# Optimization experiments

Measured on AMD Instinct MI355X. Metric: run time of the kernel, lower is better.

## Reference

```python
import jax, jax.numpy as jnp
import numpy as np


def setup_inputs() -> dict:
    key = jax.random.key(0)
    ks = jax.random.split(key, 6)
    B, S, D = 2048, 50, 128
    H, L = 8, 128
    return {
        "x": jax.random.normal(ks[0], (B, S, D), dtype=jnp.float32),
        "Wq": jax.random.normal(ks[1], (H, D, L), dtype=jnp.float32),
        "Wk": jax.random.normal(ks[2], (H, D, L), dtype=jnp.float32),
        "Wv": jax.random.normal(ks[3], (H, D, L), dtype=jnp.float32),
        "Ws": jax.random.normal(ks[4], (H, L), dtype=jnp.float32),
        "O": jax.random.normal(ks[5], (H * L, D), dtype=jnp.float32),
    }


def reference(x, Wq, Wk, Wv, Ws, O):
    # x: [B, S, D]; origin is the first node of each walk.
    B, S, D = x.shape
    H, _, L = Wq.shape
    origin = x[:, 0, :]  # [B, D]
    # key projection of origin is constant over the sequence -> compute once.
    k = jax.nn.sigmoid(jnp.einsum("bd,hdl->bhl", origin, Wk))  # [B, H, L]
    q = jax.nn.sigmoid(jnp.einsum("bsd,hdl->bshl", x, Wq))      # [B, S, H, L]
    v = jax.nn.sigmoid(jnp.einsum("bsd,hdl->bshl", x, Wv))      # [B, S, H, L]
    edge = k[:, None, :, :] * q                                  # [B, S, H, L]
    score = jnp.einsum("bshl,hl->bsh", edge, Ws)                 # [B, S, H]
    attn = jax.nn.softmax(score, axis=1)                         # softmax over walk positions
    res = jnp.einsum("bsh,bshl->bhl", attn, v)                   # [B, H, L]
    res = res.reshape(B, H * L)                                  # head-major concat (matches tf.concat)
    out = jax.nn.sigmoid(res @ O) + origin                       # [B, D]
    return out
```

## Files before the change

kernel.cpp:

```cpp
#include <hip/hip_runtime.h>
#include <hip/hip_bf16.h>


typedef _Float16 f16x8 __attribute__((ext_vector_type(8)));
typedef float f32x4 __attribute__((ext_vector_type(4)));

#define LOG2E 1.44269504088896340736f

__device__ __forceinline__ unsigned short f2h(float f) {
  _Float16 h = (_Float16)f;
  return __builtin_bit_cast(unsigned short, h);
}
__device__ __forceinline__ float h2f(unsigned short s) {
  return (float)__builtin_bit_cast(_Float16, s);
}
__device__ __forceinline__ float fexp2(float x) {
#if __has_builtin(__builtin_amdgcn_exp2f)
  return __builtin_amdgcn_exp2f(x);
#else
  return exp2f(x);
#endif
}
__device__ __forceinline__ float frcp(float x) {
#if __has_builtin(__builtin_amdgcn_rcpf)
  return __builtin_amdgcn_rcpf(x);
#else
  return 1.0f / x;
#endif
}
__device__ __forceinline__ float sig_scaled(float a) {
  return frcp(1.0f + fexp2(a));
}

__device__ __forceinline__ void dma16(const void* g, void* l) {
  __builtin_amdgcn_global_load_lds(
      (const __attribute__((address_space(1))) unsigned int*)g,
      (__attribute__((address_space(3))) unsigned int*)(unsigned int)(unsigned long long)l,
      16, 0, 0);
}

__global__ void prep_kernel(const float* __restrict__ Wq, const float* __restrict__ Wk,
                            const float* __restrict__ Wv, const float* __restrict__ O,
                            unsigned short* __restrict__ ws16) {
  const float NS = -LOG2E;
  int tid = blockIdx.x * 256 + threadIdx.x;
  for (int j = tid; j < 4 * 131072; j += 512 * 256) {
    int which = j >> 17;
    int i = j & 131071;
    float val;
    if (which == 0 || which == 2) {
      const float* W = (which == 0) ? Wq : Wv;
      int tau = i >> 11;
      int op = (i & 2047) * 2;
      int c = op >> 8;
      int o = op ^ ((c & 7) << 4);
      int k = (o & 255) >> 1;
      int n = tau * 16 + c;
      int h = n >> 7, lidx = n & 127;
      val = W[h * 16384 + k * 128 + lidx];
    } else if (which == 1) {
      int n = i >> 7, d = i & 127;
      int h = n >> 7, lidx = n & 127;
      val = Wk[h * 16384 + d * 128 + lidx];
    } else {
      int n = i >> 10, k = i & 1023;
      val = O[k * 128 + n];
    }
    ws16[j] = f2h(val * NS);
  }
}

__global__ __launch_bounds__(256, 2) void kw_kernel(
    const float* __restrict__ x, const float* __restrict__ Ws,
    const unsigned short* __restrict__ WkT, unsigned short* __restrict__ kw_all) {
  __shared__ __align__(16) char lds[16384];
  const int tid = threadIdx.x;
  const int b0 = blockIdx.x * 64;
  for (int i = tid; i < 2048; i += 256) {
    int row = i >> 5, c4 = i & 31;
    const float4 v = *(const float4*)(x + (size_t)(b0 + row) * 6400 + c4 * 4);
    uint2 pk;
    pk.x = (unsigned)f2h(v.x) | ((unsigned)f2h(v.y) << 16);
    pk.y = (unsigned)f2h(v.z) | ((unsigned)f2h(v.w) << 16);
    *(uint2*)(lds + row * 256 + ((c4 * 8) ^ ((row & 7) << 4))) = pk;
  }
  __syncthreads();
  const int w = tid >> 6, l = tid & 63, l15 = l & 15, l4 = l >> 4;
  f16x8 af[4][4];
#pragma unroll
  for (int mt = 0; mt < 4; ++mt)
#pragma unroll
    for (int kt = 0; kt < 4; ++kt) {
      int row = mt * 16 + l15;
      int c = kt * 64 + l4 * 16;
      af[mt][kt] = *(const f16x8*)(lds + row * 256 + (c ^ ((row & 7) << 4)));
    }
  const f16x8* B8 = (const f16x8*)WkT;
  for (int nt = 0; nt < 4; ++nt) {
    const int n0 = blockIdx.y * 256 + w * 64 + nt * 16;
    f16x8 bfr[4];
#pragma unroll
    for (int kt = 0; kt < 4; ++kt) bfr[kt] = B8[(size_t)(n0 + l15) * 16 + kt * 4 + l4];
    f32x4 acc[4];
#pragma unroll
    for (int mt = 0; mt < 4; ++mt) acc[mt] = (f32x4){0.f, 0.f, 0.f, 0.f};
#pragma unroll
    for (int mt = 0; mt < 4; ++mt)
#pragma unroll
      for (int kt = 0; kt < 4; ++kt)
        acc[mt] = __builtin_amdgcn_mfma_f32_16x16x32_f16(af[mt][kt], bfr[kt], acc[mt], 0, 0, 0);
    const float wsv = Ws[n0 + l15];
#pragma unroll
    for (int mt = 0; mt < 4; ++mt)
#pragma unroll
      for (int r = 0; r < 4; ++r) {
        int row = b0 + mt * 16 + l4 * 4 + r;
        kw_all[(size_t)row * 1024 + n0 + l15] = f2h(sig_scaled(acc[mt][r]) * wsv);
      }
  }
}

__global__ __launch_bounds__(256, 4) void fused_kernel(
    const float* __restrict__ x,
    const unsigned short* __restrict__ WqS, const unsigned short* __restrict__ WvS,
    const unsigned short* __restrict__ kw_all, unsigned short* __restrict__ res_all) {
  __shared__ __align__(16) char lds[32768];
  __shared__ __align__(16) unsigned short kw16[1024];
  const int tid = threadIdx.x;
  const int b = blockIdx.x;
  const int w = tid >> 6, l = tid & 63, l15 = l & 15, l4 = l >> 4;
  const int ncol = w * 256;

  const float* xb = x + (size_t)b * 6400;
#pragma unroll
  for (int j = 0; j < 8; ++j) {
    int idx = tid + j * 256;
    int row = idx >> 5, c4 = idx & 31;
    uint2 pk = {0u, 0u};
    if (row < 50) {
      const float4 v = *(const float4*)(xb + row * 128 + c4 * 4);
      pk.x = (unsigned)f2h(v.x) | ((unsigned)f2h(v.y) << 16);
      pk.y = (unsigned)f2h(v.z) | ((unsigned)f2h(v.w) << 16);
    }
    *(uint2*)(lds + row * 256 + ((c4 * 8) ^ ((row & 7) << 4))) = pk;
  }
  *(ushort4*)(kw16 + tid * 4) =
      *(const ushort4*)(kw_all + (size_t)b * 1024 + tid * 4);
  __syncthreads();

  f16x8 af[4][4];
#pragma unroll
  for (int mt = 0; mt < 4; ++mt)
#pragma unroll
    for (int kt = 0; kt < 4; ++kt) {
      int row = mt * 16 + l15;
      int c = kt * 64 + l4 * 16;
      af[mt][kt] = *(const f16x8*)(lds + row * 256 + (c ^ ((row & 7) << 4)));
    }
  __syncthreads();

  char* slot0 = lds + w * 8192;
  char* slot1 = slot0 + 4096;

  {
    const char* s = (const char*)WqS + (size_t)(ncol >> 4) * 4096 + l * 16;
    dma16(s, slot0);
    dma16(s + 1024, slot0 + 1024);
    dma16(s + 2048, slot0 + 2048);
    dma16(s + 3072, slot0 + 3072);
  }

  float pa[4][4];
#pragma unroll
  for (int mt = 0; mt < 4; ++mt)
#pragma unroll
    for (int r = 0; r < 4; ++r) pa[mt][r] = 0.f;

#pragma unroll
  for (int t = 0; t < 32; ++t) {
    const int nt = (t & 7) + ((t >> 4) << 3);
    char* cslot = (t & 1) ? slot1 : slot0;
    char* nslot = (t & 1) ? slot0 : slot1;
    if (t < 31) {
      const int t1 = t + 1;
      const int nt1 = (t1 & 7) + ((t1 >> 4) << 3);
      const unsigned short* W1 = ((t1 >> 3) & 1) ? WvS : WqS;
      const char* s = (const char*)W1 + (size_t)((ncol >> 4) + nt1) * 4096 + l * 16;
      dma16(s, nslot);
      dma16(s + 1024, nslot + 1024);
      dma16(s + 2048, nslot + 2048);
      dma16(s + 3072, nslot + 3072);
      asm volatile("s_waitcnt vmcnt(4)" ::: "memory");
    } else {
      asm volatile("s_waitcnt vmcnt(0)" ::: "memory");
    }
    f32x4 acc[4];
#pragma unroll
    for (int mt = 0; mt < 4; ++mt) acc[mt] = (f32x4){0.f, 0.f, 0.f, 0.f};
    {
      f16x8 bf0, bf1;
      {
        int o0 = (l15 * 256 + 0 * 64 + l4 * 16) ^ ((l15 & 7) << 4);
        int o1 = (l15 * 256 + 1 * 64 + l4 * 16) ^ ((l15 & 7) << 4);
        bf0 = *(const f16x8*)(cslot + o0);
        bf1 = *(const f16x8*)(cslot + o1);
      }
#pragma unroll
      for (int mt = 0; mt < 4; ++mt)
        acc[mt] = __builtin_amdgcn_mfma_f32_16x16x32_f16(af[mt][0], bf0, acc[mt], 0, 0, 0);
#pragma unroll
      for (int mt = 0; mt < 4; ++mt)
        acc[mt] = __builtin_amdgcn_mfma_f32_16x16x32_f16(af[mt][1], bf1, acc[mt], 0, 0, 0);
      {
        int o2 = (l15 * 256 + 2 * 64 + l4 * 16) ^ ((l15 & 7) << 4);
        int o3 = (l15 * 256 + 3 * 64 + l4 * 16) ^ ((l15 & 7) << 4);
        bf0 = *(const f16x8*)(cslot + o2);
        bf1 = *(const f16x8*)(cslot + o3);
      }
#pragma unroll
      for (int mt = 0; mt < 4; ++mt)
        acc[mt] = __builtin_amdgcn_mfma_f32_16x16x32_f16(af[mt][2], bf0, acc[mt], 0, 0, 0);
#pragma unroll
      for (int mt = 0; mt < 4; ++mt)
        acc[mt] = __builtin_amdgcn_mfma_f32_16x16x32_f16(af[mt][3], bf1, acc[mt], 0, 0, 0);
    }

    if (((t >> 3) & 1) == 0) {
      const float kwv = h2f(kw16[ncol + nt * 16 + l15]);
#pragma unroll
      for (int mt = 0; mt < 4; ++mt)
#pragma unroll
        for (int r = 0; r < 4; ++r) {
          if (mt < 3 || r < 2)
            pa[mt][r] = fmaf(sig_scaled(acc[mt][r]), kwv, pa[mt][r]);
        }
      if ((t & 7) == 7) {
#pragma unroll
        for (int mt = 0; mt < 4; ++mt)
#pragma unroll
          for (int r = 0; r < 4; ++r) {
            if (mt == 3 && r >= 2) continue;
            float v = pa[mt][r];
            v += __shfl_xor(v, 1);
            v += __shfl_xor(v, 2);
            v += __shfl_xor(v, 4);
            v += __shfl_xor(v, 8);
            pa[mt][r] = v;
          }
        float m = -3.0e38f;
#pragma unroll
        for (int mt = 0; mt < 4; ++mt)
#pragma unroll
          for (int r = 0; r < 4; ++r) {
            if (mt == 3 && r >= 2) continue;
            int row = mt * 16 + l4 * 4 + r;
            m = fmaxf(m, (row < 50) ? pa[mt][r] : -3.0e38f);
          }
        m = fmaxf(m, __shfl_xor(m, 16));
        m = fmaxf(m, __shfl_xor(m, 32));
        float tsum = 0.f;
#pragma unroll
        for (int mt = 0; mt < 4; ++mt)
#pragma unroll
          for (int r = 0; r < 4; ++r) {
            int row = mt * 16 + l4 * 4 + r;
            float e = (row < 50 && !(mt == 3 && r >= 2))
                          ? fexp2((pa[mt][r] - m) * LOG2E) : 0.f;
            pa[mt][r] = e;
            tsum += e;
          }
        tsum += __shfl_xor(tsum, 16);
        tsum += __shfl_xor(tsum, 32);
        const float rs = frcp(tsum);
#pragma unroll
        for (int mt = 0; mt < 4; ++mt)
#pragma unroll
          for (int r = 0; r < 4; ++r) pa[mt][r] *= rs;
      }
    } else {
      float part = 0.f;
#pragma unroll
      for (int mt = 0; mt < 4; ++mt)
#pragma unroll
        for (int r = 0; r < 4; ++r) {
          if (mt < 3 || r < 2)
            part = fmaf(pa[mt][r], sig_scaled(acc[mt][r]), part);
        }
      part += __shfl_xor(part, 16);
      part += __shfl_xor(part, 32);
      if (l < 16)
        res_all[(size_t)b * 1024 + ncol + nt * 16 + l15] = f2h(part);
      if (t == 15) {
#pragma unroll
        for (int mt = 0; mt < 4; ++mt)
#pragma unroll
          for (int r = 0; r < 4; ++r) pa[mt][r] = 0.f;
      }
    }
  }
}

__global__ __launch_bounds__(256, 4) void out_kernel(
    const unsigned short* __restrict__ res_all, const unsigned short* __restrict__ OT,
    const float* __restrict__ x, float* __restrict__ out) {
  const int tid = threadIdx.x;
  const int w = tid >> 6, l = tid & 63, l15 = l & 15, l4 = l >> 4;
  const int b0 = blockIdx.x * 16;
  const f16x8* A8 = (const f16x8*)res_all;
  const f16x8* B8 = (const f16x8*)OT;
  f32x4 acc0 = (f32x4){0.f, 0.f, 0.f, 0.f};
  f32x4 acc1 = (f32x4){0.f, 0.f, 0.f, 0.f};
  const int n0 = w * 32;
#pragma unroll 4
  for (int kt = 0; kt < 32; ++kt) {
    f16x8 a = A8[(size_t)(b0 + l15) * 128 + kt * 4 + l4];
    f16x8 bq0 = B8[(size_t)(n0 + l15) * 128 + kt * 4 + l4];
    f16x8 bq1 = B8[(size_t)(n0 + 16 + l15) * 128 + kt * 4 + l4];
    acc0 = __builtin_amdgcn_mfma_f32_16x16x32_f16(a, bq0, acc0, 0, 0, 0);
    acc1 = __builtin_amdgcn_mfma_f32_16x16x32_f16(a, bq1, acc1, 0, 0, 0);
  }
#pragma unroll
  for (int r = 0; r < 4; ++r) {
    int row = b0 + l4 * 4 + r;
    int col0 = n0 + l15;
    int col1 = n0 + 16 + l15;
    out[(size_t)row * 128 + col0] = sig_scaled(acc0[r]) + x[(size_t)row * 6400 + col0];
    out[(size_t)row * 128 + col1] = sig_scaled(acc1[r]) + x[(size_t)row * 6400 + col1];
  }
}

extern "C" void kernel_launch(void* const* d_in, const int* in_sizes, int n_in,
                              void* d_out, int out_size, void* d_ws, size_t ws_size,
                              hipStream_t stream) {
  const float* x  = (const float*)d_in[0];
  const float* Wq = (const float*)d_in[1];
  const float* Wk = (const float*)d_in[2];
  const float* Wv = (const float*)d_in[3];
  const float* Ws = (const float*)d_in[4];
  const float* O  = (const float*)d_in[5];
  float* out = (float*)d_out;

  unsigned short* ws16    = (unsigned short*)d_ws;
  unsigned short* WqS     = ws16;
  unsigned short* WkT     = ws16 + 131072;
  unsigned short* WvS     = ws16 + 262144;
  unsigned short* OT      = ws16 + 393216;
  unsigned short* kw_all  = ws16 + 524288;
  unsigned short* res_all = ws16 + 524288 + 2097152;

  prep_kernel<<<512, 256, 0, stream>>>(Wq, Wk, Wv, O, ws16);
  kw_kernel<<<dim3(32, 4), 256, 0, stream>>>(x, Ws, WkT, kw_all);
  fused_kernel<<<2048, 256, 0, stream>>>(x, WqS, WvS, kw_all, res_all);
  out_kernel<<<128, 256, 0, stream>>>(res_all, OT, x, out);
}
```

Baseline: 129.6 us.

## Triple-buffer weight tile DMA with prefetch distance two and MFMA priority

```diff
diff --git a/kernel.cpp b/kernel.cpp
--- a/kernel.cpp
+++ b/kernel.cpp
@@ -120,11 +120,11 @@
   }
 }
 
-__global__ __launch_bounds__(256, 4) void fused_kernel(
+__global__ __launch_bounds__(256, 3) void fused_kernel(
     const float* __restrict__ x,
     const unsigned short* __restrict__ WqS, const unsigned short* __restrict__ WvS,
     const unsigned short* __restrict__ kw_all, unsigned short* __restrict__ res_all) {
-  __shared__ __align__(16) char lds[32768];
+  __shared__ __align__(16) char lds[49152];
   __shared__ __align__(16) unsigned short kw16[1024];
   const int tid = threadIdx.x;
   const int b = blockIdx.x;
@@ -159,15 +159,20 @@
     }
   __syncthreads();
 
-  char* slot0 = lds + w * 8192;
-  char* slot1 = slot0 + 4096;
+  char* slotb = lds + w * 12288;
 
   {
-    const char* s = (const char*)WqS + (size_t)(ncol >> 4) * 4096 + l * 16;
-    dma16(s, slot0);
-    dma16(s + 1024, slot0 + 1024);
-    dma16(s + 2048, slot0 + 2048);
-    dma16(s + 3072, slot0 + 3072);
+    const char* s0 = (const char*)WqS + (size_t)(ncol >> 4) * 4096 + l * 16;
+    dma16(s0, slotb);
+    dma16(s0 + 1024, slotb + 1024);
+    dma16(s0 + 2048, slotb + 2048);
+    dma16(s0 + 3072, slotb + 3072);
+    const char* s1 = s0 + 4096;
+    char* n1 = slotb + 4096;
+    dma16(s1, n1);
+    dma16(s1 + 1024, n1 + 1024);
+    dma16(s1 + 2048, n1 + 2048);
+    dma16(s1 + 3072, n1 + 3072);
   }
 
   float pa[4][4];
@@ -179,21 +184,24 @@
 #pragma unroll
   for (int t = 0; t < 32; ++t) {
     const int nt = (t & 7) + ((t >> 4) << 3);
-    char* cslot = (t & 1) ? slot1 : slot0;
-    char* nslot = (t & 1) ? slot0 : slot1;
-    if (t < 31) {
-      const int t1 = t + 1;
-      const int nt1 = (t1 & 7) + ((t1 >> 4) << 3);
-      const unsigned short* W1 = ((t1 >> 3) & 1) ? WvS : WqS;
-      const char* s = (const char*)W1 + (size_t)((ncol >> 4) + nt1) * 4096 + l * 16;
+    char* cslot = slotb + (t % 3) * 4096;
+    if (t < 30) {
+      const int t2 = t + 2;
+      const int nt2 = (t2 & 7) + ((t2 >> 4) << 3);
+      const unsigned short* W2 = ((t2 >> 3) & 1) ? WvS : WqS;
+      const char* s = (const char*)W2 + (size_t)((ncol >> 4) + nt2) * 4096 + l * 16;
+      char* nslot = slotb + (t2 % 3) * 4096;
       dma16(s, nslot);
       dma16(s + 1024, nslot + 1024);
       dma16(s + 2048, nslot + 2048);
       dma16(s + 3072, nslot + 3072);
+      asm volatile("s_waitcnt vmcnt(8)" ::: "memory");
+    } else if (t == 30) {
       asm volatile("s_waitcnt vmcnt(4)" ::: "memory");
     } else {
       asm volatile("s_waitcnt vmcnt(0)" ::: "memory");
     }
+    __builtin_amdgcn_s_setprio(1);
     f32x4 acc[4];
 #pragma unroll
     for (int mt = 0; mt < 4; ++mt) acc[mt] = (f32x4){0.f, 0.f, 0.f, 0.f};
@@ -224,6 +232,7 @@
       for (int mt = 0; mt < 4; ++mt)
         acc[mt] = __builtin_amdgcn_mfma_f32_16x16x32_f16(af[mt][3], bf1, acc[mt], 0, 0, 0);
     }
+    __builtin_amdgcn_s_setprio(0);
 
     if (((t >> 3) & 1) == 0) {
       const float kwv = h2f(kw16[ncol + nt * 16 + l15]);
```

Result: faster. 124.5 us (-3.9%).
